# Kernel optimization log

Measured on AMD Instinct MI355X. Metric: run time of the kernel, lower is better.

Reference implementation:

```python
import jax, jax.numpy as jnp
import numpy as np

N_NODES = 100_000
N_EDGES = 500_000
D = 256      # node_dim == embed_dim
T = 256      # time_dim
ED = 256     # edge_dim
EMB = 256
B = 2048
K = 10       # n_neighbors fanout
H = 8        # attention heads
QD = D + T           # query dim = node feat || time emb
KD = EMB + T + ED    # key dim = nbr emb || time emb || edge feat


def setup_inputs() -> dict:
    key = jax.random.key(0)
    ks = jax.random.split(key, 24)
    s = 0.05
    nrm = lambda k, sh: jax.random.normal(k, sh, jnp.float32) * s
    inp = {}
    inp['memory'] = nrm(ks[0], (N_NODES, D))
    inp['node_features'] = nrm(ks[1], (N_NODES, D))
    inp['edge_features'] = nrm(ks[2], (N_EDGES, ED))
    inp['time_w'] = nrm(ks[3], (T,))
    inp['time_b'] = nrm(ks[4], (T,))
    # stacked per-layer attention params (layer 0 and layer 1 share shapes since node_dim==embed_dim)
    inp['Wq'] = nrm(ks[5], (2, QD, QD)); inp['bq'] = jnp.zeros((2, QD), jnp.float32)
    inp['Wk'] = nrm(ks[6], (2, KD, QD)); inp['bk'] = jnp.zeros((2, QD), jnp.float32)
    inp['Wv'] = nrm(ks[7], (2, KD, QD)); inp['bv'] = jnp.zeros((2, QD), jnp.float32)
    inp['Wo'] = nrm(ks[8], (2, QD, QD)); inp['bo'] = jnp.zeros((2, QD), jnp.float32)
    inp['W1'] = nrm(ks[9], (2, QD + EMB, EMB)); inp['b1'] = jnp.zeros((2, EMB), jnp.float32)
    inp['W2'] = nrm(ks[10], (2, EMB, EMB)); inp['b2'] = jnp.zeros((2, EMB), jnp.float32)
    inp['timestamps'] = jax.random.uniform(ks[11], (B,), jnp.float32, 100.0, 200.0)
    inp['edge_times1'] = jax.random.uniform(ks[12], (B, K), jnp.float32, 0.0, 100.0)
    inp['edge_times2'] = jax.random.uniform(ks[13], (B * K, K), jnp.float32, 0.0, 100.0)
    inp['src_nodes'] = jax.random.randint(ks[14], (B,), 0, N_NODES)
    inp['neighbors1'] = jax.random.randint(ks[15], (B, K), 0, N_NODES)
    inp['edge_idx1'] = jax.random.randint(ks[16], (B, K), 0, N_EDGES)
    inp['neighbors2'] = jax.random.randint(ks[17], (B * K, K), 0, N_NODES)
    inp['edge_idx2'] = jax.random.randint(ks[18], (B * K, K), 0, N_EDGES)
    return inp


def reference(memory, node_features, edge_features, time_w, time_b,
              Wq, bq, Wk, bk, Wv, bv, Wo, bo, W1, b1, W2, b2,
              timestamps, edge_times1, edge_times2,
              src_nodes, neighbors1, edge_idx1, neighbors2, edge_idx2):
    te = lambda t: jnp.cos(t[..., None] * time_w + time_b)  # TimeEncode: cos(w*t + b)

    def attn(i, src_feat, nbr_emb, edge_t_emb, edge_feat, mask):
        # src_feat [Bn,D]; nbr_emb [Bn,K,D]; edge_t_emb [Bn,K,T]; edge_feat [Bn,K,ED]; mask [Bn,K] (True = padded, neighbor==0)
        Bn = src_feat.shape[0]
        q = jnp.concatenate([src_feat, te(jnp.zeros((Bn,), src_feat.dtype))], -1)   # [Bn,QD]
        k = jnp.concatenate([nbr_emb, edge_t_emb, edge_feat], -1)                  # [Bn,K,KD]
        dh = QD // H
        qh = (q @ Wq[i] + bq[i]).reshape(Bn, H, dh)
        kh = (k @ Wk[i] + bk[i]).reshape(Bn, -1, H, dh)
        vh = (k @ Wv[i] + bv[i]).reshape(Bn, -1, H, dh)
        scores = jnp.einsum('bhd,bkhd->bhk', qh, kh) / jnp.sqrt(jnp.asarray(dh, q.dtype))
        scores = jnp.where(mask[:, None, :], -1e9, scores)
        o = jnp.einsum('bhk,bkhd->bhd', jax.nn.softmax(scores, axis=-1), vh).reshape(Bn, QD)
        o = o @ Wo[i] + bo[i]
        o = jnp.where(jnp.all(mask, -1)[:, None], 0.0, o)  # fully-padded neighborhoods -> 0
        h = jax.nn.relu(jnp.concatenate([o, src_feat], -1) @ W1[i] + b1[i])  # MergeLayer fc1
        return h @ W2[i] + b2[i]

    # ---- layer-0 (raw) features: memory[n] + node_features[n] ----
    f_src0 = memory[src_nodes] + node_features[src_nodes]           # [B,D]
    n1f = neighbors1.reshape(-1)                                    # [B*K]
    f_n1_0 = memory[n1f] + node_features[n1f]                       # [B*K,D]
    dt1 = te(timestamps[:, None] - edge_times1)                     # [B,K,T]
    m1 = neighbors1 == 0
    ef1 = edge_features[edge_idx1]                                  # [B,K,ED]
    # ---- layer-1 embedding of source nodes (attn[0]) ----
    src_l1 = attn(0, f_src0, f_n1_0.reshape(B, K, -1), dt1, ef1, m1)
    # ---- layer-1 embedding of hop-1 neighbors using hop-2 samples (attn[0]) ----
    ts_rep = jnp.repeat(timestamps, K)                              # [B*K]
    n2f = neighbors2.reshape(-1)
    f_n2_0 = memory[n2f] + node_features[n2f]                       # [B*K*K,D]
    dt2 = te(ts_rep[:, None] - edge_times2)                         # [B*K,K,T]
    m2 = neighbors2 == 0
    n1_l1 = attn(0, f_n1_0, f_n2_0.reshape(B * K, K, -1), dt2, edge_features[edge_idx2], m2)
    # ---- layer-2 embedding of source nodes (attn[1]) ----
    return attn(1, src_l1, n1_l1.reshape(B, K, -1), dt1, ef1, m1)   # [B,EMB]
```

## Files before the change

kernel.cpp:

```cpp
#include <hip/hip_runtime.h>
#include <hip/hip_bf16.h>
#include <math.h>

#define BB 2048
#define KK 10
#define N1R 20480
#define Q2T 22528
#define NNODES 100000

typedef short short4v __attribute__((ext_vector_type(4)));
typedef short short8 __attribute__((ext_vector_type(8)));
typedef float f32x4 __attribute__((ext_vector_type(4)));

__device__ __forceinline__ float bf2f(short s) {
  union { unsigned u; float f; } x;
  x.u = ((unsigned)(unsigned short)s) << 16;
  return x.f;
}
__device__ __forceinline__ short f2bf(float f) {
  union { float f; unsigned u; } x;
  x.f = f;
  unsigned r = x.u + 0x7fffu + ((x.u >> 16) & 1u);
  return (short)(r >> 16);
}

#define FALL_BLKS 25000
#define PW_BLKS   14336
#define SM_BLKS   10
#define RED_BLKS  384

__global__ __launch_bounds__(256) void mega_prep_kernel(
    short* __restrict__ WqT, short* __restrict__ WkvT, short* __restrict__ WoC,
    short* __restrict__ W1T, short* __restrict__ W1P, short* __restrict__ W2T,
    short* __restrict__ WkQ,
    float* __restrict__ bkv, float* __restrict__ zbias,
    float* __restrict__ qconst, float* __restrict__ b1p, short* __restrict__ f_all,
    const float* __restrict__ Wq, const float* __restrict__ Wk, const float* __restrict__ Wv,
    const float* __restrict__ Wo, const float* __restrict__ W1, const float* __restrict__ W2,
    const float* __restrict__ bk, const float* __restrict__ bv, const float* __restrict__ bq,
    const float* __restrict__ bo, const float* __restrict__ b1,
    const float* __restrict__ tb, const float* __restrict__ mem, const float* __restrict__ nf)
{
  int b = blockIdx.x;
  int tid = threadIdx.x;
  if (b < FALL_BLKS) {
    int row = b * 4 + (tid >> 6);
    int c = (tid & 63) * 4;
    f32x4 a = *(const f32x4*)(mem + (size_t)row*256 + c);
    f32x4 d = *(const f32x4*)(nf  + (size_t)row*256 + c);
    short4v o;
#pragma unroll
    for (int e = 0; e < 4; ++e) o[e] = f2bf(a[e] + d[e]);
    *(short4v*)(f_all + (size_t)row*256 + c) = o;
  } else if (b < FALL_BLKS + PW_BLKS) {
    const int PER = 512*256 + 1024*768 + 512*512 + 256*768 + 256*256 + 768*512;
    int idx = (b - FALL_BLKS) * 256 + tid;
    if (idx >= 2 * PER) return;
    int i = idx / PER, r = idx % PER;
    const int S1 = 512*256, S2 = S1 + 1024*768, S3 = S2 + 512*512, S4 = S3 + 256*768,
              S5 = S4 + 256*256;
    if (r < S1) {
      int n = r >> 8, k = r & 255;
      WqT[(size_t)i*S1 + r] = f2bf(Wq[(size_t)i*262144 + (size_t)k*512 + n]);
    } else if (r < S2) {
      int rr = r - S1; int n = rr / 768, k = rr % 768;
      float v = (n < 512) ? Wk[(size_t)i*393216 + (size_t)k*512 + n]
                          : Wv[(size_t)i*393216 + (size_t)k*512 + (n - 512)];
      WkvT[(size_t)i*786432 + rr] = f2bf(v);
    } else if (r < S3) {
      int rr = r - S2;
      WoC[(size_t)i*262144 + rr] = f2bf(Wo[(size_t)i*262144 + rr]);
    } else if (r < S4) {
      int rr = r - S3; int n = rr / 768, k = rr % 768;
      short v = f2bf(W1[(size_t)i*196608 + (size_t)k*256 + n]);
      W1T[(size_t)i*196608 + rr] = v;
      if (k >= 512) W1P[(size_t)i*196608 + rr] = v;
    } else if (r < S5) {
      int rr = r - S4; int n = rr >> 8, k = rr & 255;
      W2T[(size_t)i*65536 + rr] = f2bf(W2[(size_t)i*65536 + (size_t)k*256 + n]);
    } else {
      int rr = r - S5; int c = rr >> 9, n = rr & 511, h = n >> 6, d = n & 63;
      WkQ[(size_t)i*393216 + (size_t)h*49152 + (size_t)c*64 + d] =
          f2bf(Wk[(size_t)i*393216 + (size_t)c*512 + n]);
    }
  } else if (b < FALL_BLKS + PW_BLKS + SM_BLKS) {
    int idx = (b - FALL_BLKS - PW_BLKS) * 256 + tid;
    if (idx < 2048) {
      int i = idx >> 10, n = idx & 1023;
      bkv[idx] = (n < 512) ? bk[i*512 + n] : bv[i*512 + (n - 512)];
    } else if (idx < 2560) {
      zbias[idx - 2048] = 0.f;
    }
  } else {
    int w = (b - FALL_BLKS - PW_BLKS - SM_BLKS) * 4 + (tid >> 6);
    int lane = tid & 63;
    if (w < 1024) {
      int i = w >> 9, n = w & 511;
      float acc = 0.f;
#pragma unroll
      for (int tt = 0; tt < 4; ++tt) {
        int t = lane + tt * 64;
        acc += cosf(tb[t]) * Wq[(size_t)i*262144 + (size_t)(256 + t)*512 + n];
      }
#pragma unroll
      for (int s = 1; s < 64; s <<= 1) acc += __shfl_xor(acc, s);
      if (lane == 0) qconst[w] = acc + bq[i*512 + n];
    } else if (w < 1536) {
      int r = w - 1024;
      int i = r >> 8, n = r & 255;
      float acc = 0.f;
#pragma unroll
      for (int dd = 0; dd < 8; ++dd) {
        int d = lane + dd * 64;
        acc += bo[i*512 + d] * W1[(size_t)i*196608 + (size_t)d*256 + n];
      }
#pragma unroll
      for (int s = 1; s < 64; s <<= 1) acc += __shfl_xor(acc, s);
      if (lane == 0) b1p[r] = acc + b1[i*256 + n];
    }
  }
}

__global__ __launch_bounds__(256) void build_feats_kernel(
    short* __restrict__ f_src, short* __restrict__ f_n1, const short* __restrict__ f_all,
    const int* __restrict__ src_nodes, const int* __restrict__ n1)
{
  int row = blockIdx.x * 4 + (threadIdx.x >> 6);
  int c = (threadIdx.x & 63) * 4;
  int node; short* dst;
  if (row < BB) { node = src_nodes[row]; dst = f_src + (size_t)row * 256; }
  else { node = n1[row - BB]; dst = f_n1 + (size_t)(row - BB) * 256; }
  *(short4v*)(dst + c) = *(const short4v*)(f_all + (size_t)node*256 + c);
}

template<bool RELU, bool OUTF32>
__global__ __launch_bounds__(256) void gemm128(
    int M, int N, int Kd,
    const short* __restrict__ A1, int lda1, int ksplit,
    const short* __restrict__ A2, int lda2,
    const short* __restrict__ Bt,
    const float* __restrict__ bias,
    short* __restrict__ outB, float* __restrict__ outF, int ldo)
{
  __shared__ short As[128][72];
  __shared__ short Bs[128][72];
  const int nbj = N >> 7;
  const int bi = blockIdx.x / nbj;
  const int bj = blockIdx.x % nbj;
  const int tid = threadIdx.x;
  const int lane = tid & 63;
  const int wave = tid >> 6;
  const int wr = (wave >> 1) * 64;
  const int wc = (wave & 1) * 64;

  f32x4 acc[4][4];
  const f32x4 zv = {0.f, 0.f, 0.f, 0.f};
#pragma unroll
  for (int m = 0; m < 4; ++m)
#pragma unroll
    for (int n = 0; n < 4; ++n) acc[m][n] = zv;

  const size_t arow0 = (size_t)bi * 128;
  const short* Brow = Bt + (size_t)bj * 128 * (size_t)Kd;

  for (int kt = 0; kt < Kd; kt += 64) {
#pragma unroll
    for (int it = 0; it < 4; ++it) {
      int chunk = tid + it * 256;
      int row = chunk >> 3;
      int c16 = (chunk & 7) * 8;
      int gk = kt + c16;
      const short* srcA;
      if (gk < ksplit) srcA = A1 + (arow0 + row) * (size_t)lda1 + gk;
      else             srcA = A2 + (arow0 + row) * (size_t)lda2 + (gk - ksplit);
      *(short8*)&As[row][c16] = *(const short8*)srcA;
      *(short8*)&Bs[row][c16] = *(const short8*)(Brow + (size_t)row * Kd + kt + c16);
    }
    __syncthreads();
#pragma unroll
    for (int kk = 0; kk < 64; kk += 32) {
      short8 af[4], bfr[4];
#pragma unroll
      for (int m = 0; m < 4; ++m)
        af[m] = *(const short8*)&As[wr + m*16 + (lane & 15)][kk + (lane >> 4) * 8];
#pragma unroll
      for (int n = 0; n < 4; ++n)
        bfr[n] = *(const short8*)&Bs[wc + n*16 + (lane & 15)][kk + (lane >> 4) * 8];
#pragma unroll
      for (int m = 0; m < 4; ++m)
#pragma unroll
        for (int n = 0; n < 4; ++n)
          acc[m][n] = __builtin_amdgcn_mfma_f32_16x16x32_bf16(af[m], bfr[n], acc[m][n], 0, 0, 0);
    }
    __syncthreads();
  }

#pragma unroll
  for (int m = 0; m < 4; ++m) {
#pragma unroll
    for (int r = 0; r < 4; ++r) {
      size_t row = arow0 + wr + m*16 + ((lane >> 4) * 4 + r);
#pragma unroll
      for (int n = 0; n < 4; ++n) {
        int col = bj*128 + wc + n*16 + (lane & 15);
        float v = acc[m][n][r] + bias[col];
        if (RELU) v = v > 0.f ? v : 0.f;
        if (OUTF32) outF[row * (size_t)ldo + col] = v;
        else        outB[row * (size_t)ldo + col] = f2bf(v);
      }
    }
  }
}

__global__ __launch_bounds__(256) void qk_gemm_kernel(
    const short* __restrict__ qh, const short* __restrict__ WkQh,
    short* __restrict__ qk)
{
  __shared__ short As[128][72];
  __shared__ short Bs[128][72];
  const int bi = blockIdx.x / 6;
  const int bj = blockIdx.x % 6;
  const int h = blockIdx.y;
  const int tid = threadIdx.x;
  const int lane = tid & 63;
  const int wave = tid >> 6;
  const int wr = (wave >> 1) * 64;
  const int wc = (wave & 1) * 64;

  f32x4 acc[4][4];
  const f32x4 zv = {0.f, 0.f, 0.f, 0.f};
#pragma unroll
  for (int m = 0; m < 4; ++m)
#pragma unroll
    for (int n = 0; n < 4; ++n) acc[m][n] = zv;

#pragma unroll
  for (int it = 0; it < 4; ++it) {
    int chunk = tid + it * 256;
    int row = chunk >> 3;
    int c16 = (chunk & 7) * 8;
    *(short8*)&As[row][c16] = *(const short8*)(qh + (size_t)(bi*128 + row) * 512 + h*64 + c16);
    *(short8*)&Bs[row][c16] = *(const short8*)(WkQh + (size_t)h*49152 + (size_t)(bj*128 + row)*64 + c16);
  }
  __syncthreads();
#pragma unroll
  for (int kk = 0; kk < 64; kk += 32) {
    short8 af[4], bfr[4];
#pragma unroll
    for (int m = 0; m < 4; ++m)
      af[m] = *(const short8*)&As[wr + m*16 + (lane & 15)][kk + (lane >> 4) * 8];
#pragma unroll
    for (int n = 0; n < 4; ++n)
      bfr[n] = *(const short8*)&Bs[wc + n*16 + (lane & 15)][kk + (lane >> 4) * 8];
#pragma unroll
    for (int m = 0; m < 4; ++m)
#pragma unroll
      for (int n = 0; n < 4; ++n)
        acc[m][n] = __builtin_amdgcn_mfma_f32_16x16x32_bf16(af[m], bfr[n], acc[m][n], 0, 0, 0);
  }

#pragma unroll
  for (int m = 0; m < 4; ++m) {
#pragma unroll
    for (int r = 0; r < 4; ++r) {
      size_t row = (size_t)bi*128 + wr + m*16 + ((lane >> 4) * 4 + r);
#pragma unroll
      for (int n = 0; n < 4; ++n) {
        int col = bj*128 + wc + n*16 + (lane & 15);
        qk[row * 6144 + (size_t)h * 768 + col] = f2bf(acc[m][n][r]);
      }
    }
  }
}

template<int MODE>
__global__ __launch_bounds__(256) void attn_mix3_kernel(
    const short* __restrict__ qk_l, const short* __restrict__ tab,
    const int* __restrict__ nb1, const float* __restrict__ et1, const int* __restrict__ ei1,
    const int* __restrict__ nb2, const float* __restrict__ et2, const int* __restrict__ ei2,
    const float* __restrict__ ts,
    const float* __restrict__ tw, const float* __restrict__ tb,
    const float* __restrict__ ef,
    short* __restrict__ kbar_l, int q0)
{
  int lq = blockIdx.x * 4 + (threadIdx.x >> 6);
  int gq = q0 + lq;
  int lane = threadIdx.x & 63;
  int c4 = lane * 4;

  f32x4 tw4 = *(const f32x4*)(tw + c4);
  f32x4 tb4 = *(const f32x4*)(tb + c4);

  const int* nbp; const float* etp; const int* eip; float tsq;
  if (MODE == 0) {
    nbp = nb1 + gq*10; etp = et1 + gq*10; eip = ei1 + gq*10; tsq = ts[gq];
  } else {
    if (gq < BB) { nbp = nb1 + gq*10; etp = et1 + gq*10; eip = ei1 + gq*10; tsq = ts[gq]; }
    else {
      int q2 = gq - BB;
      nbp = nb2 + q2*10; etp = et2 + q2*10; eip = ei2 + q2*10; tsq = ts[q2/10];
    }
  }

  int nb[10]; int nmask = 0;
#pragma unroll
  for (int j = 0; j < 10; ++j) { nb[j] = nbp[j]; nmask += (nb[j] == 0); }

  float kr[10][12];
#pragma unroll
  for (int j = 0; j < 10; ++j) {
    int gi = (MODE == 0) ? (gq*10 + j) : nb[j];
    short4v a = *(const short4v*)(tab + (size_t)gi*256 + c4);
    float dt = tsq - etp[j];
    f32x4 e4 = *(const f32x4*)(ef + (size_t)eip[j]*256 + c4);
#pragma unroll
    for (int e = 0; e < 4; ++e) {
      kr[j][e]     = bf2f(a[e]);
      kr[j][4 + e] = cosf(dt * tw4[e] + tb4[e]);
      kr[j][8 + e] = e4[e];
    }
  }

  const short* qkb = qk_l + (size_t)lq * 6144;
  short* kbb = kbar_l + (size_t)lq * 6144;
  bool zero = (nmask == 10);

#pragma unroll
  for (int h = 0; h < 8; ++h) {
    float qv[12];
    {
      short4v a = *(const short4v*)(qkb + h*768 + c4);
      short4v b = *(const short4v*)(qkb + h*768 + 256 + c4);
      short4v c = *(const short4v*)(qkb + h*768 + 512 + c4);
#pragma unroll
      for (int e = 0; e < 4; ++e) {
        qv[e]     = bf2f(a[e]);
        qv[4 + e] = bf2f(b[e]);
        qv[8 + e] = bf2f(c[e]);
      }
    }
    float s[10];
#pragma unroll
    for (int j = 0; j < 10; ++j) {
      float d = 0.f;
#pragma unroll
      for (int e = 0; e < 12; ++e) d += qv[e] * kr[j][e];
      d += __shfl_xor(d, 1);  d += __shfl_xor(d, 2);  d += __shfl_xor(d, 4);
      d += __shfl_xor(d, 8);  d += __shfl_xor(d, 16); d += __shfl_xor(d, 32);
      s[j] = (nb[j] == 0) ? -1e9f : d * 0.125f;
    }
    float mx = s[0];
#pragma unroll
    for (int j = 1; j < 10; ++j) mx = fmaxf(mx, s[j]);
    float p[10], sum = 0.f;
#pragma unroll
    for (int j = 0; j < 10; ++j) { p[j] = __expf(s[j] - mx); sum += p[j]; }
    float inv = 1.f / sum;

    short4v o0, o1, o2;
#pragma unroll
    for (int e = 0; e < 4; ++e) {
      float v0 = 0.f, v1 = 0.f, v2 = 0.f;
#pragma unroll
      for (int j = 0; j < 10; ++j) {
        float pj = p[j];
        v0 += pj * kr[j][e];
        v1 += pj * kr[j][4 + e];
        v2 += pj * kr[j][8 + e];
      }
      o0[e] = zero ? (short)0 : f2bf(v0 * inv);
      o1[e] = zero ? (short)0 : f2bf(v1 * inv);
      o2[e] = zero ? (short)0 : f2bf(v2 * inv);
    }
    *(short4v*)(kbb + h*768 + c4)       = o0;
    *(short4v*)(kbb + h*768 + 256 + c4) = o1;
    *(short4v*)(kbb + h*768 + 512 + c4) = o2;
  }
}

__global__ __launch_bounds__(256) void gemm_n64_kernel(
    int M, int Kd,
    const short* __restrict__ A, int lda,
    const short* __restrict__ Bt,
    const float* __restrict__ bias,
    short* __restrict__ out, int ldo)
{
  __shared__ short As[128][72];
  __shared__ short Bs[64][72];
  const int bi = blockIdx.x;
  const int h = blockIdx.y;
  const int tid = threadIdx.x;
  const int lane = tid & 63;
  const int wave = tid >> 6;

  const short* Ah = A + (size_t)h * 768;
  const short* Bh = Bt + (size_t)h * 64 * (size_t)Kd;
  const float* biash = bias + h * 64;
  short* outh = out + h * 64;

  f32x4 acc[2][4];
  const f32x4 zv = {0.f, 0.f, 0.f, 0.f};
#pragma unroll
  for (int m = 0; m < 2; ++m)
#pragma unroll
    for (int n = 0; n < 4; ++n) acc[m][n] = zv;

  const size_t arow0 = (size_t)bi * 128;
  for (int kt = 0; kt < Kd; kt += 64) {
#pragma unroll
    for (int it = 0; it < 4; ++it) {
      int chunk = tid + it * 256;
      int row = chunk >> 3;
      int c16 = (chunk & 7) * 8;
      *(short8*)&As[row][c16] = *(const short8*)(Ah + (arow0 + row) * (size_t)lda + kt + c16);
    }
#pragma unroll
    for (int it = 0; it < 2; ++it) {
      int chunk = tid + it * 256;
      int row = chunk >> 3;
      int c16 = (chunk & 7) * 8;
      *(short8*)&Bs[row][c16] = *(const short8*)(Bh + (size_t)row * Kd + kt + c16);
    }
    __syncthreads();
#pragma unroll
    for (int kk = 0; kk < 64; kk += 32) {
      short8 af[2], bfr[4];
#pragma unroll
      for (int m = 0; m < 2; ++m)
        af[m] = *(const short8*)&As[wave*32 + m*16 + (lane & 15)][kk + (lane >> 4) * 8];
#pragma unroll
      for (int n = 0; n < 4; ++n)
        bfr[n] = *(const short8*)&Bs[n*16 + (lane & 15)][kk + (lane >> 4) * 8];
#pragma unroll
      for (int m = 0; m < 2; ++m)
#pragma unroll
        for (int n = 0; n < 4; ++n)
          acc[m][n] = __builtin_amdgcn_mfma_f32_16x16x32_bf16(af[m], bfr[n], acc[m][n], 0, 0, 0);
    }
    __syncthreads();
  }

#pragma unroll
  for (int m = 0; m < 2; ++m) {
#pragma unroll
    for (int r = 0; r < 4; ++r) {
      size_t row = arow0 + wave*32 + m*16 + ((lane >> 4) * 4 + r);
#pragma unroll
      for (int n = 0; n < 4; ++n) {
        int col = n*16 + (lane & 15);
        outh[row * (size_t)ldo + col] = f2bf(acc[m][n][r] + biash[col]);
      }
    }
  }
}

extern "C" void kernel_launch(void* const* d_in, const int* in_sizes, int n_in,
                              void* d_out, int out_size, void* d_ws, size_t ws_size,
                              hipStream_t stream)
{
  const float* memory   = (const float*)d_in[0];
  const float* node_f   = (const float*)d_in[1];
  const float* edge_f   = (const float*)d_in[2];
  const float* time_w   = (const float*)d_in[3];
  const float* time_b   = (const float*)d_in[4];
  const float* Wq = (const float*)d_in[5];
  const float* bq = (const float*)d_in[6];
  const float* Wk = (const float*)d_in[7];
  const float* bk = (const float*)d_in[8];
  const float* Wv = (const float*)d_in[9];
  const float* bv = (const float*)d_in[10];
  const float* Wo = (const float*)d_in[11];
  const float* bo = (const float*)d_in[12];
  const float* W1 = (const float*)d_in[13];
  const float* b1 = (const float*)d_in[14];
  const float* W2 = (const float*)d_in[15];
  const float* b2 = (const float*)d_in[16];
  const float* timestamps = (const float*)d_in[17];
  const float* et1 = (const float*)d_in[18];
  const float* et2 = (const float*)d_in[19];
  const int* src_nodes  = (const int*)d_in[20];
  const int* neighbors1 = (const int*)d_in[21];
  const int* edge_idx1  = (const int*)d_in[22];
  const int* neighbors2 = (const int*)d_in[23];
  const int* edge_idx2  = (const int*)d_in[24];
  float* out = (float*)d_out;

  char* wsp = (char*)d_ws;
  size_t off = 0;
  auto alloc = [&](size_t bytes) -> void* {
    void* p = wsp + off;
    off += (bytes + 255) & ~(size_t)255;
    return p;
  };
  short* WqT  = (short*)alloc((size_t)2*512*256*2);
  short* WkvT = (short*)alloc((size_t)2*1024*768*2);
  short* WoC  = (short*)alloc((size_t)2*512*512*2);
  short* W1T  = (short*)alloc((size_t)2*256*768*2);
  short* W1P  = (short*)alloc((size_t)2*256*768*2);
  short* W2T  = (short*)alloc((size_t)2*256*256*2);
  short* WkQ  = (short*)alloc((size_t)2*768*512*2);
  float* qconst = (float*)alloc(2*512*4);
  float* bkv    = (float*)alloc(2*1024*4);
  float* b1p    = (float*)alloc(2*256*4);
  float* zbias  = (float*)alloc(512*4);
  short* f_all  = (short*)alloc((size_t)NNODES*256*2);
  short* f_src  = (short*)alloc((size_t)BB*256*2);
  short* f_n1   = (short*)alloc((size_t)N1R*256*2);
  short* src_l1 = (short*)alloc((size_t)BB*256*2);
  short* n1_l1  = (short*)alloc((size_t)N1R*256*2);
  short* qh     = (short*)alloc((size_t)Q2T*512*2);
  short* obuf   = (short*)alloc((size_t)Q2T*512*2);
  short* hbuf   = (short*)alloc((size_t)Q2T*256*2);
  size_t fixed = off;

  int CB = 2048;
  {
    const int cands[3] = {5632, 2816, 2048};
    for (int c = 0; c < 3; ++c) {
      size_t need = fixed
        + (((size_t)cands[c]*6144*2 + 255) & ~(size_t)255)
        + (((size_t)cands[c]*6144*2 + 255) & ~(size_t)255);
      if (need <= ws_size) { CB = cands[c]; break; }
    }
  }
  short* qkbuf = (short*)alloc((size_t)CB*6144*2);
  short* kbar  = (short*)alloc((size_t)CB*6144*2);

  auto g128 = [&](int M, int N, int Kd,
                  const short* A1, int lda1, int ksplit, const short* A2, int lda2,
                  const short* Bt, const float* bias,
                  short* outB, float* outF, int ldo, int mode) {
    dim3 grid((unsigned)((M/128) * (N/128))), blk(256);
    if (mode == 0)      gemm128<false,false><<<grid, blk, 0, stream>>>(M,N,Kd,A1,lda1,ksplit,A2,lda2,Bt,bias,outB,outF,ldo);
    else if (mode == 1) gemm128<true ,false><<<grid, blk, 0, stream>>>(M,N,Kd,A1,lda1,ksplit,A2,lda2,Bt,bias,outB,outF,ldo);
    else                gemm128<false,true ><<<grid, blk, 0, stream>>>(M,N,Kd,A1,lda1,ksplit,A2,lda2,Bt,bias,outB,outF,ldo);
  };

  mega_prep_kernel<<<dim3(FALL_BLKS + PW_BLKS + SM_BLKS + RED_BLKS), dim3(256), 0, stream>>>(
      WqT, WkvT, WoC, W1T, W1P, W2T, WkQ, bkv, zbias, qconst, b1p, f_all,
      Wq, Wk, Wv, Wo, W1, W2, bk, bv, bq, bo, b1, time_b, memory, node_f);
  build_feats_kernel<<<dim3(Q2T/4), dim3(256), 0, stream>>>(f_src, f_n1, f_all, src_nodes, neighbors1);
  g128(256, 512, 512, W1T,          768, 512, W1T,          768, WoC,          zbias, W1P,          nullptr, 768, 0);
  g128(256, 512, 512, W1T + 196608, 768, 512, W1T + 196608, 768, WoC + 262144, zbias, W1P + 196608, nullptr, 768, 0);

  g128(Q2T, 512, 256, f_src, 256, 256, f_src, 256, WqT, qconst, qh, nullptr, 512, 0);
  for (int b0 = 0; b0 < Q2T; b0 += CB) {
    qk_gemm_kernel<<<dim3((CB/128)*6, 8), dim3(256), 0, stream>>>(
        qh + (size_t)b0*512, WkQ, qkbuf);
    attn_mix3_kernel<1><<<dim3(CB/4), dim3(256), 0, stream>>>(
        qkbuf, f_all, neighbors1, et1, edge_idx1, neighbors2, et2, edge_idx2,
        timestamps, time_w, time_b, edge_f, kbar, b0);
    gemm_n64_kernel<<<dim3(CB/128, 8), dim3(256), 0, stream>>>(
        CB, 768, kbar, 6144, WkvT + 512*768, bkv + 512, obuf + (size_t)b0*512, 512);
  }
  g128(Q2T, 256, 768, obuf, 512, 512, f_src, 256, W1P, b1p, hbuf, nullptr, 256, 1);
  g128(Q2T, 256, 256, hbuf, 256, 256, hbuf, 256, W2T, b2, src_l1, nullptr, 256, 0);

  g128(BB, 512, 256, src_l1, 256, 256, src_l1, 256, WqT + 512*256, qconst + 512, qh, nullptr, 512, 0);
  qk_gemm_kernel<<<dim3((BB/128)*6, 8), dim3(256), 0, stream>>>(qh, WkQ + 393216, qkbuf);
  attn_mix3_kernel<0><<<dim3(BB/4), dim3(256), 0, stream>>>(
      qkbuf, n1_l1, neighbors1, et1, edge_idx1, neighbors1, et1, edge_idx1,
      timestamps, time_w, time_b, edge_f, kbar, 0);
  gemm_n64_kernel<<<dim3(BB/128, 8), dim3(256), 0, stream>>>(
      BB, 768, kbar, 6144, WkvT + 786432 + 512*768, bkv + 1024 + 512, obuf, 512);
  g128(BB, 256, 768, obuf, 512, 512, src_l1, 256, W1P + 196608, b1p + 256, hbuf, nullptr, 256, 1);
  g128(BB, 256, 256, hbuf, 256, 256, hbuf, 256, W2T + 65536, b2 + 256, nullptr, out, 256, 3);
}
```

Before: 829.6 us.

## Fuse MLP GEMMs, merge feature gather into prep, batch Wo-W1 GEMMs, enlarge chunk

Merges build_feats into the prep kernel: the gathered features are computed directly from fp32 memory and node_features rather than re-read from f_all. Fuses the two MLP GEMMs (W1 with ReLU, then W2) into one kernel that keeps the hidden tile in shared memory, removing the hbuf round trip. Combines the two per-layer Wo·W1 precompute GEMMs into one launch by choosing the B matrix per row tile. Adds larger chunk-size candidates so the attention loop can run in fewer iterations when workspace allows. The fused MLP kernel uses about 125KB of shared memory with 128 output rows per block, which gives few blocks and low occupancy.

```diff
diff --git a/kernel.cpp b/kernel.cpp
--- a/kernel.cpp
+++ b/kernel.cpp
@@ -25,6 +25,7 @@
 }
 
 #define FALL_BLKS 25000
+#define FEAT_BLKS 5632
 #define PW_BLKS   14336
 #define SM_BLKS   10
 #define RED_BLKS  384
@@ -35,6 +36,8 @@
     short* __restrict__ WkQ,
     float* __restrict__ bkv, float* __restrict__ zbias,
     float* __restrict__ qconst, float* __restrict__ b1p, short* __restrict__ f_all,
+    short* __restrict__ f_src, short* __restrict__ f_n1,
+    const int* __restrict__ src_nodes, const int* __restrict__ n1,
     const float* __restrict__ Wq, const float* __restrict__ Wk, const float* __restrict__ Wv,
     const float* __restrict__ Wo, const float* __restrict__ W1, const float* __restrict__ W2,
     const float* __restrict__ bk, const float* __restrict__ bv, const float* __restrict__ bq,
@@ -52,9 +55,21 @@
 #pragma unroll
     for (int e = 0; e < 4; ++e) o[e] = f2bf(a[e] + d[e]);
     *(short4v*)(f_all + (size_t)row*256 + c) = o;
-  } else if (b < FALL_BLKS + PW_BLKS) {
+  } else if (b < FALL_BLKS + FEAT_BLKS) {
+    int row = (b - FALL_BLKS) * 4 + (tid >> 6);
+    int c = (tid & 63) * 4;
+    int node; short* dst;
+    if (row < BB) { node = src_nodes[row]; dst = f_src + (size_t)row * 256; }
+    else { node = n1[row - BB]; dst = f_n1 + (size_t)(row - BB) * 256; }
+    f32x4 a = *(const f32x4*)(mem + (size_t)node*256 + c);
+    f32x4 d = *(const f32x4*)(nf  + (size_t)node*256 + c);
+    short4v o;
+#pragma unroll
+    for (int e = 0; e < 4; ++e) o[e] = f2bf(a[e] + d[e]);
+    *(short4v*)(dst + c) = o;
+  } else if (b < FALL_BLKS + FEAT_BLKS + PW_BLKS) {
     const int PER = 512*256 + 1024*768 + 512*512 + 256*768 + 256*256 + 768*512;
-    int idx = (b - FALL_BLKS) * 256 + tid;
+    int idx = (b - FALL_BLKS - FEAT_BLKS) * 256 + tid;
     if (idx >= 2 * PER) return;
     int i = idx / PER, r = idx % PER;
     const int S1 = 512*256, S2 = S1 + 1024*768, S3 = S2 + 512*512, S4 = S3 + 256*768,
@@ -83,8 +98,8 @@
       WkQ[(size_t)i*393216 + (size_t)h*49152 + (size_t)c*64 + d] =
           f2bf(Wk[(size_t)i*393216 + (size_t)c*512 + n]);
     }
-  } else if (b < FALL_BLKS + PW_BLKS + SM_BLKS) {
-    int idx = (b - FALL_BLKS - PW_BLKS) * 256 + tid;
+  } else if (b < FALL_BLKS + FEAT_BLKS + PW_BLKS + SM_BLKS) {
+    int idx = (b - FALL_BLKS - FEAT_BLKS - PW_BLKS) * 256 + tid;
     if (idx < 2048) {
       int i = idx >> 10, n = idx & 1023;
       bkv[idx] = (n < 512) ? bk[i*512 + n] : bv[i*512 + (n - 512)];
@@ -92,7 +107,7 @@
       zbias[idx - 2048] = 0.f;
     }
   } else {
-    int w = (b - FALL_BLKS - PW_BLKS - SM_BLKS) * 4 + (tid >> 6);
+    int w = (b - FALL_BLKS - FEAT_BLKS - PW_BLKS - SM_BLKS) * 4 + (tid >> 6);
     int lane = tid & 63;
     if (w < 1024) {
       int i = w >> 9, n = w & 511;
@@ -121,24 +136,12 @@
   }
 }
 
-__global__ __launch_bounds__(256) void build_feats_kernel(
-    short* __restrict__ f_src, short* __restrict__ f_n1, const short* __restrict__ f_all,
-    const int* __restrict__ src_nodes, const int* __restrict__ n1)
-{
-  int row = blockIdx.x * 4 + (threadIdx.x >> 6);
-  int c = (threadIdx.x & 63) * 4;
-  int node; short* dst;
-  if (row < BB) { node = src_nodes[row]; dst = f_src + (size_t)row * 256; }
-  else { node = n1[row - BB]; dst = f_n1 + (size_t)(row - BB) * 256; }
-  *(short4v*)(dst + c) = *(const short4v*)(f_all + (size_t)node*256 + c);
-}
-
 template<bool RELU, bool OUTF32>
 __global__ __launch_bounds__(256) void gemm128(
     int M, int N, int Kd,
     const short* __restrict__ A1, int lda1, int ksplit,
     const short* __restrict__ A2, int lda2,
-    const short* __restrict__ Bt,
+    const short* __restrict__ Bt, const short* __restrict__ Bt2, int msplitB,
     const float* __restrict__ bias,
     short* __restrict__ outB, float* __restrict__ outF, int ldo)
 {
@@ -161,7 +164,8 @@
     for (int n = 0; n < 4; ++n) acc[m][n] = zv;
 
   const size_t arow0 = (size_t)bi * 128;
-  const short* Brow = Bt + (size_t)bj * 128 * (size_t)Kd;
+  const short* Bsel = (bi * 128 < msplitB) ? Bt : Bt2;
+  const short* Brow = Bsel + (size_t)bj * 128 * (size_t)Kd;
 
   for (int kt = 0; kt < Kd; kt += 64) {
 #pragma unroll
@@ -449,6 +453,128 @@
       for (int n = 0; n < 4; ++n) {
         int col = n*16 + (lane & 15);
         outh[row * (size_t)ldo + col] = f2bf(acc[m][n][r] + biash[col]);
+      }
+    }
+  }
+}
+
+template<bool OUTF32>
+__global__ __launch_bounds__(256) void w12_kernel(
+    const short* __restrict__ A1,
+    const short* __restrict__ A2,
+    const short* __restrict__ B1,
+    const float* __restrict__ bias1,
+    const short* __restrict__ B2,
+    const float* __restrict__ bias2,
+    short* __restrict__ outB, float* __restrict__ outF)
+{
+  __shared__ short As[128][72];
+  __shared__ short Bs[256][72];
+  __shared__ short C1[128][280];
+  const int tid = threadIdx.x;
+  const int lane = tid & 63;
+  const int wave = tid >> 6;
+  const int wr = (wave >> 1) * 64;
+  const int wc = (wave & 1) * 128;
+  const size_t arow0 = (size_t)blockIdx.x * 128;
+
+  f32x4 acc[4][8];
+  const f32x4 zv = {0.f, 0.f, 0.f, 0.f};
+#pragma unroll
+  for (int m = 0; m < 4; ++m)
+#pragma unroll
+    for (int n = 0; n < 8; ++n) acc[m][n] = zv;
+
+  for (int kt = 0; kt < 768; kt += 64) {
+#pragma unroll
+    for (int it = 0; it < 4; ++it) {
+      int chunk = tid + it * 256;
+      int row = chunk >> 3;
+      int c16 = (chunk & 7) * 8;
+      int gk = kt + c16;
+      const short* srcA;
+      if (gk < 512) srcA = A1 + (arow0 + row) * 512 + gk;
+      else          srcA = A2 + (arow0 + row) * 256 + (gk - 512);
+      *(short8*)&As[row][c16] = *(const short8*)srcA;
+    }
+#pragma unroll
+    for (int it = 0; it < 8; ++it) {
+      int chunk = tid + it * 256;
+      int row = chunk >> 3;
+      int c16 = (chunk & 7) * 8;
+      *(short8*)&Bs[row][c16] = *(const short8*)(B1 + (size_t)row * 768 + kt + c16);
+    }
+    __syncthreads();
+#pragma unroll
+    for (int kk = 0; kk < 64; kk += 32) {
+      short8 af[4], bfr[8];
+#pragma unroll
+      for (int m = 0; m < 4; ++m)
+        af[m] = *(const short8*)&As[wr + m*16 + (lane & 15)][kk + (lane >> 4) * 8];
+#pragma unroll
+      for (int n = 0; n < 8; ++n)
+        bfr[n] = *(const short8*)&Bs[wc + n*16 + (lane & 15)][kk + (lane >> 4) * 8];
+#pragma unroll
+      for (int m = 0; m < 4; ++m)
+#pragma unroll
+        for (int n = 0; n < 8; ++n)
+          acc[m][n] = __builtin_amdgcn_mfma_f32_16x16x32_bf16(af[m], bfr[n], acc[m][n], 0, 0, 0);
+    }
+    __syncthreads();
+  }
+#pragma unroll
+  for (int m = 0; m < 4; ++m) {
+#pragma unroll
+    for (int r = 0; r < 4; ++r) {
+      int row = wr + m*16 + ((lane >> 4) * 4 + r);
+#pragma unroll
+      for (int n = 0; n < 8; ++n) {
+        int col = wc + n*16 + (lane & 15);
+        float v = acc[m][n][r] + bias1[col];
+        C1[row][col] = f2bf(v > 0.f ? v : 0.f);
+        acc[m][n][r] = 0.f;
+      }
+    }
+  }
+  __syncthreads();
+
+  for (int kt = 0; kt < 256; kt += 64) {
+#pragma unroll
+    for (int it = 0; it < 8; ++it) {
+      int chunk = tid + it * 256;
+      int row = chunk >> 3;
+      int c16 = (chunk & 7) * 8;
+      *(short8*)&Bs[row][c16] = *(const short8*)(B2 + (size_t)row * 256 + kt + c16);
+    }
+    __syncthreads();
+#pragma unroll
+    for (int kk = 0; kk < 64; kk += 32) {
+      short8 af[4], bfr[8];
+#pragma unroll
+      for (int m = 0; m < 4; ++m)
+        af[m] = *(const short8*)&C1[wr + m*16 + (lane & 15)][kt + kk + (lane >> 4) * 8];
+#pragma unroll
+      for (int n = 0; n < 8; ++n)
+        bfr[n] = *(const short8*)&Bs[wc + n*16 + (lane & 15)][kk + (lane >> 4) * 8];
+#pragma unroll
+      for (int m = 0; m < 4; ++m)
+#pragma unroll
+        for (int n = 0; n < 8; ++n)
+          acc[m][n] = __builtin_amdgcn_mfma_f32_16x16x32_bf16(af[m], bfr[n], acc[m][n], 0, 0, 0);
+    }
+    __syncthreads();
+  }
+#pragma unroll
+  for (int m = 0; m < 4; ++m) {
+#pragma unroll
+    for (int r = 0; r < 4; ++r) {
+      size_t row = arow0 + wr + m*16 + ((lane >> 4) * 4 + r);
+#pragma unroll
+      for (int n = 0; n < 8; ++n) {
+        int col = wc + n*16 + (lane & 15);
+        float v = acc[m][n][r] + bias2[col];
+        if (OUTF32) outF[row * 256 + col] = v;
+        else        outB[row * 256 + col] = f2bf(v);
       }
     }
   }
@@ -510,13 +636,12 @@
   short* n1_l1  = (short*)alloc((size_t)N1R*256*2);
   short* qh     = (short*)alloc((size_t)Q2T*512*2);
   short* obuf   = (short*)alloc((size_t)Q2T*512*2);
-  short* hbuf   = (short*)alloc((size_t)Q2T*256*2);
   size_t fixed = off;
 
   int CB = 2048;
   {
-    const int cands[3] = {5632, 2816, 2048};
-    for (int c = 0; c < 3; ++c) {
+    const int cands[5] = {22528, 11264, 5632, 2816, 2048};
+    for (int c = 0; c < 5; ++c) {
       size_t need = fixed
         + (((size_t)cands[c]*6144*2 + 255) & ~(size_t)255)
         + (((size_t)cands[c]*6144*2 + 255) & ~(size_t)255);
@@ -526,24 +651,16 @@
   short* qkbuf = (short*)alloc((size_t)CB*6144*2);
   short* kbar  = (short*)alloc((size_t)CB*6144*2);
 
-  auto g128 = [&](int M, int N, int Kd,
-                  const short* A1, int lda1, int ksplit, const short* A2, int lda2,
-                  const short* Bt, const float* bias,
-                  short* outB, float* outF, int ldo, int mode) {
-    dim3 grid((unsigned)((M/128) * (N/128))), blk(256);
-    if (mode == 0)      gemm128<false,false><<<grid, blk, 0, stream>>>(M,N,Kd,A1,lda1,ksplit,A2,lda2,Bt,bias,outB,outF,ldo);
-    else if (mode == 1) gemm128<true ,false><<<grid, blk, 0, stream>>>(M,N,Kd,A1,lda1,ksplit,A2,lda2,Bt,bias,outB,outF,ldo);
-    else                gemm128<false,true ><<<grid, blk, 0, stream>>>(M,N,Kd,A1,lda1,ksplit,A2,lda2,Bt,bias,outB,outF,ldo);
-  };
-
-  mega_prep_kernel<<<dim3(FALL_BLKS + PW_BLKS + SM_BLKS + RED_BLKS), dim3(256), 0, stream>>>(
+  const int BIG = 1 << 30;
+  mega_prep_kernel<<<dim3(FALL_BLKS + FEAT_BLKS + PW_BLKS + SM_BLKS + RED_BLKS), dim3(256), 0, stream>>>(
       WqT, WkvT, WoC, W1T, W1P, W2T, WkQ, bkv, zbias, qconst, b1p, f_all,
+      f_src, f_n1, src_nodes, neighbors1,
       Wq, Wk, Wv, Wo, W1, W2, bk, bv, bq, bo, b1, time_b, memory, node_f);
-  build_feats_kernel<<<dim3(Q2T/4), dim3(256), 0, stream>>>(f_src, f_n1, f_all, src_nodes, neighbors1);
-  g128(256, 512, 512, W1T,          768, 512, W1T,          768, WoC,          zbias, W1P,          nullptr, 768, 0);
-  g128(256, 512, 512, W1T + 196608, 768, 512, W1T + 196608, 768, WoC + 262144, zbias, W1P + 196608, nullptr, 768, 0);
-
-  g128(Q2T, 512, 256, f_src, 256, 256, f_src, 256, WqT, qconst, qh, nullptr, 512, 0);
+  gemm128<false,false><<<dim3(16), dim3(256), 0, stream>>>(
+      512, 512, 512, W1T, 768, 512, W1T, 768, WoC, WoC + 262144, 256, zbias, W1P, nullptr, 768);
+
+  gemm128<false,false><<<dim3((Q2T/128)*4), dim3(256), 0, stream>>>(
+      Q2T, 512, 256, f_src, 256, 256, f_src, 256, WqT, WqT, BIG, qconst, qh, nullptr, 512);
   for (int b0 = 0; b0 < Q2T; b0 += CB) {
     qk_gemm_kernel<<<dim3((CB/128)*6, 8), dim3(256), 0, stream>>>(
         qh + (size_t)b0*512, WkQ, qkbuf);
@@ -553,16 +670,18 @@
     gemm_n64_kernel<<<dim3(CB/128, 8), dim3(256), 0, stream>>>(
         CB, 768, kbar, 6144, WkvT + 512*768, bkv + 512, obuf + (size_t)b0*512, 512);
   }
-  g128(Q2T, 256, 768, obuf, 512, 512, f_src, 256, W1P, b1p, hbuf, nullptr, 256, 1);
-  g128(Q2T, 256, 256, hbuf, 256, 256, hbuf, 256, W2T, b2, src_l1, nullptr, 256, 0);
-
-  g128(BB, 512, 256, src_l1, 256, 256, src_l1, 256, WqT + 512*256, qconst + 512, qh, nullptr, 512, 0);
+  w12_kernel<false><<<dim3(Q2T/128), dim3(256), 0, stream>>>(
+      obuf, f_src, W1P, b1p, W2T, b2, src_l1, nullptr);
+
+  gemm128<false,false><<<dim3((BB/128)*4), dim3(256), 0, stream>>>(
+      BB, 512, 256, src_l1, 256, 256, src_l1, 256, WqT + 512*256, WqT + 512*256, BIG,
+      qconst + 512, qh, nullptr, 512);
   qk_gemm_kernel<<<dim3((BB/128)*6, 8), dim3(256), 0, stream>>>(qh, WkQ + 393216, qkbuf);
   attn_mix3_kernel<0><<<dim3(BB/4), dim3(256), 0, stream>>>(
       qkbuf, n1_l1, neighbors1, et1, edge_idx1, neighbors1, et1, edge_idx1,
       timestamps, time_w, time_b, edge_f, kbar, 0);
   gemm_n64_kernel<<<dim3(BB/128, 8), dim3(256), 0, stream>>>(
       BB, 768, kbar, 6144, WkvT + 786432 + 512*768, bkv + 1024 + 512, obuf, 512);
-  g128(BB, 256, 768, obuf, 512, 512, src_l1, 256, W1P + 196608, b1p + 256, hbuf, nullptr, 256, 1);
-  g128(BB, 256, 256, hbuf, 256, 256, hbuf, 256, W2T + 65536, b2 + 256, nullptr, out, 256, 3);
-}
+  w12_kernel<true><<<dim3(BB/128), dim3(256), 0, stream>>>(
+      obuf, src_l1, W1P + 196608, b1p + 256, W2T + 65536, b2 + 256, nullptr, out);
+}
```

Measured after the change: 775.1 us. -6.6%, faster.
